# Optimization experiments

Hardware: AMD Instinct MI355X
Metric: run time of the kernel (lower is better)

## Reference

```python
import jax, jax.numpy as jnp
import numpy as np

N = 512
H = 128
L = 4
NUM_RBF = 50
CUTOFF = 5.0
NMOL = 16
OUT = 1


def setup_inputs() -> dict:
    key = jax.random.key(0)
    ks = jax.random.split(key, 12)
    s = lambda f: 1.0 / np.sqrt(f)
    atomic_numbers = jax.random.randint(ks[0], (N,), 0, 100)
    positions = jax.random.normal(ks[1], (N, 3), dtype=jnp.float32) * 2.0
    batch = jnp.sort(jax.random.randint(ks[2], (N,), 0, NMOL))
    return {
        'atomic_numbers': atomic_numbers,
        'positions': positions,
        'batch': batch,
        'embed': jax.random.normal(ks[3], (100, H), dtype=jnp.float32) * 0.1,
        'msg_w1': jax.random.normal(ks[4], (L, H + NUM_RBF + 3, H), dtype=jnp.float32) * s(H + NUM_RBF + 3),
        'msg_b1': jnp.zeros((L, H), jnp.float32),
        'msg_w2': jax.random.normal(ks[5], (L, H, H), dtype=jnp.float32) * s(H),
        'msg_b2': jnp.zeros((L, H), jnp.float32),
        'upd_w1': jax.random.normal(ks[6], (L, 2 * H, H), dtype=jnp.float32) * s(2 * H),
        'upd_b1': jnp.zeros((L, H), jnp.float32),
        'upd_w2': jax.random.normal(ks[7], (L, H, H), dtype=jnp.float32) * s(H),
        'upd_b2': jnp.zeros((L, H), jnp.float32),
        'out_w1': jax.random.normal(ks[8], (H, H // 2), dtype=jnp.float32) * s(H),
        'out_b1': jnp.zeros((H // 2,), jnp.float32),
        'out_w2': jax.random.normal(ks[9], (H // 2, OUT), dtype=jnp.float32) * s(H // 2),
        'out_b2': jnp.zeros((OUT,), jnp.float32),
    }


def _forward(atomic_numbers, positions, batch, embed, msg_w1, msg_b1, msg_w2,
             msg_b2, upd_w1, upd_b1, upd_w2, upd_b2, out_w1, out_b1, out_w2, out_b2):
    x = embed[jnp.clip(atomic_numbers, 0, 99)]                      # [N,H]
    # all-pairs geometry: row i = source, col j = target (matches repeat_interleave/repeat)
    diff = positions[:, None, :] - positions[None, :, :]            # [N,N,3]
    dist = jnp.linalg.norm(diff, axis=-1)                           # [N,N]
    not_self = jnp.arange(N)[:, None] != jnp.arange(N)[None, :]
    valid = (dist < CUTOFF) & not_self                              # [N,N] edge mask
    dirs = diff / jnp.maximum(dist, 1e-8)[..., None]                # [N,N,3]
    # gaussian RBF: centers linspace(0, cutoff, num_rbf), width = cutoff/num_rbf
    centers = jnp.linspace(0.0, CUTOFF, NUM_RBF)
    width = CUTOFF / NUM_RBF
    rbf = jnp.exp(-(dist[..., None] - centers) ** 2 / (2.0 * width ** 2))  # [N,N,50]

    for l in range(L):
        # Linear over concat([x_j, rbf, dirs]) split by input blocks (same math)
        Wx = msg_w1[l, :H]
        Wr = msg_w1[l, H:H + NUM_RBF]
        Wd = msg_w1[l, H + NUM_RBF:]
        pre = (x @ Wx)[:, None, :] \
            + jnp.einsum('ijr,rh->ijh', rbf, Wr) \
            + jnp.einsum('ijd,dh->ijh', dirs, Wd) + msg_b1[l]       # [N,N,H]
        m = jax.nn.silu(pre) @ msg_w2[l] + msg_b2[l]                # [N,N,H]
        m = jnp.where(valid[..., None], m, 0.0)
        aggr = m.sum(axis=0)                                        # scatter-add to target j
        upd_in = jnp.concatenate([x, aggr], axis=-1)                # [N,2H]
        x = x + jax.nn.silu(upd_in @ upd_w1[l] + upd_b1[l]) @ upd_w2[l] + upd_b2[l]

    # per-molecule mean pool
    sums = jax.ops.segment_sum(x, batch, num_segments=NMOL)         # [NMOL,H]
    counts = jax.ops.segment_sum(jnp.ones((N,), x.dtype), batch, num_segments=NMOL)
    pooled = sums / jnp.maximum(counts, 1.0)[:, None]
    return jax.nn.silu(pooled @ out_w1 + out_b1) @ out_w2 + out_b2  # [NMOL,OUT]


def reference(atomic_numbers, positions, batch, embed, msg_w1, msg_b1, msg_w2,
              msg_b2, upd_w1, upd_b1, upd_w2, upd_b2, out_w1, out_b1, out_w2, out_b2):
    return _forward(atomic_numbers, positions, batch, embed, msg_w1, msg_b1, msg_w2,
                    msg_b2, upd_w1, upd_b1, upd_w2, upd_b2, out_w1, out_b1, out_w2, out_b2)
```

## Files before the change

### kernel.cpp

```cpp
#include <hip/hip_runtime.h>
#include <math.h>

#define N 512
#define H 128
#define L 4
#define NUM_RBF 50
#define NMOL 16
#define SUPER 64
#define FSTRIDE 72

typedef __attribute__((ext_vector_type(8))) short short8;
typedef __attribute__((ext_vector_type(4))) float float4v;
typedef __attribute__((ext_vector_type(4))) int int4v;

__device__ __forceinline__ float silu_f(float v) {
    return v / (1.0f + __expf(-v));
}

__device__ __forceinline__ unsigned short f2bf(float f) {
    unsigned int u = __float_as_uint(f);
    unsigned int r = (u + 0x7FFFu + ((u >> 16) & 1u)) >> 16;
    return (unsigned short)r;
}

__global__ __launch_bounds__(512) void k_embed_lin(const int* __restrict__ an,
                                                   const float* __restrict__ embed,
                                                   const float* __restrict__ pos,
                                                   const float* __restrict__ wx,
                                                   const float* __restrict__ b1,
                                                   float* __restrict__ x,
                                                   float* __restrict__ a,
                                                   int* __restrict__ nbr,
                                                   int* __restrict__ ncnt) {
    int j = blockIdx.x;
    int tid = threadIdx.x;
    int lane = tid & 63;
    int wave = tid >> 6;
    int h = tid & 127;
    int grp = tid >> 7;

    __shared__ float xs[H];
    __shared__ int wsum8[8];
    __shared__ float part[4][H];

    float pjx = pos[j * 3 + 0], pjy = pos[j * 3 + 1], pjz = pos[j * 3 + 2];

    if (tid < H) {
        int z = an[j];
        z = min(max(z, 0), 99);
        float xv = embed[z * H + tid];
        xs[tid] = xv;
        x[j * H + tid] = xv;
    }

    {
        int i = tid;
        float dx = pos[i * 3 + 0] - pjx;
        float dy = pos[i * 3 + 1] - pjy;
        float dz = pos[i * 3 + 2] - pjz;
        float d2 = dx * dx + dy * dy + dz * dz;
        int valid = (d2 < 25.0f) && (i != j);
        unsigned long long m = __ballot(valid);
        int pre = __popcll(m & ((1ull << lane) - 1ull));
        if (lane == 0) wsum8[wave] = __popcll(m);
        __syncthreads();
        int wbase = 0, total = 0;
        for (int w = 0; w < 8; w++) {
            if (w < wave) wbase += wsum8[w];
            total += wsum8[w];
        }
        if (valid) nbr[j * 512 + wbase + pre] = i;
        int padded = (total + 63) & ~63;
        for (int s = total + tid; s < padded; s += 512) nbr[j * 512 + s] = j;
        if (tid == 0) ncnt[j] = total;
    }

    {
        float p0 = 0.f, p1 = 0.f, p2 = 0.f, p3 = 0.f;
        int k0 = grp * 32;
#pragma unroll 8
        for (int k = 0; k < 32; k += 4) {
            p0 += xs[k0 + k]     * wx[(k0 + k)     * H + h];
            p1 += xs[k0 + k + 1] * wx[(k0 + k + 1) * H + h];
            p2 += xs[k0 + k + 2] * wx[(k0 + k + 2) * H + h];
            p3 += xs[k0 + k + 3] * wx[(k0 + k + 3) * H + h];
        }
        part[grp][h] = (p0 + p1) + (p2 + p3);
    }
    __syncthreads();
    if (grp == 0)
        a[j * H + h] = part[0][h] + part[1][h] + part[2][h] + part[3][h] + b1[h];
}

__global__ __launch_bounds__(512) void k_layer(const float* __restrict__ a,
                                               const float* __restrict__ pos,
                                               const int* __restrict__ nbr,
                                               const int* __restrict__ ncnt,
                                               const float* __restrict__ wfeat,
                                               const float* __restrict__ w2,
                                               const float* __restrict__ b2,
                                               const float* __restrict__ u1,
                                               const float* __restrict__ ub1,
                                               const float* __restrict__ u2,
                                               const float* __restrict__ ub2,
                                               float* __restrict__ x,
                                               const float* __restrict__ wxn,
                                               const float* __restrict__ b1n,
                                               float* __restrict__ a_next) {
    int j = blockIdx.x;
    int tid = threadIdx.x;
    int g = tid >> 8;
    int t8 = tid & 255;
    int lane = tid & 63;
    int wv4 = (tid >> 6) & 3;
    int nn = lane & 15;
    int quad = lane >> 4;
    int hbase = wv4 * 32;

    __shared__ unsigned short F[2][2][SUPER * FSTRIDE];
    __shared__ int nidx[2][2][SUPER];
    __shared__ float sjp[2][H];
    __shared__ float sj[H], xj[H], ag[H], hid[H], xn[H];
    __shared__ float part[4][H];

    int cnt = ncnt[j];
    float pjx = pos[j * 3 + 0], pjy = pos[j * 3 + 1], pjz = pos[j * 3 + 2];

    if (tid < 2 * H) sjp[tid >> 7][tid & 127] = 0.0f;
    if (tid < H) xj[tid] = x[j * H + tid];

    short8 bfrag[2][2];
    for (int c = 0; c < 2; c++) {
        for (int t = 0; t < 2; t++) {
            short8 b;
            int h = hbase + 16 * t + nn;
#pragma unroll
            for (int jj = 0; jj < 8; jj++) {
                int k = c * 32 + quad * 8 + jj;
                float v = (k < NUM_RBF + 3) ? wfeat[k * H + h] : 0.0f;
                b[jj] = (short)f2bf(v);
            }
            bfrag[c][t] = b;
        }
    }

    const float DELTA = 5.0f / 49.0f;
    float pacc0 = 0.0f, pacc1 = 0.0f;

    int S = (cnt + 63) >> 6;
    int rounds = (S + 1) >> 1;

    int il = t8 >> 2;
    int kb = (t8 & 3) * 16;

    auto stage = [&](int s, int b) {
        int ni = nbr[j * 512 + s * 64 + il];
        if ((t8 & 3) == 0) nidx[g][b][il] = ni;
        float dx = pos[ni * 3 + 0] - pjx;
        float dy = pos[ni * 3 + 1] - pjy;
        float dz = pos[ni * 3 + 2] - pjz;
        float d = sqrtf(dx * dx + dy * dy + dz * dz);
        float rinv = 1.0f / fmaxf(d, 1e-8f);
        unsigned short vals[16];
#pragma unroll
        for (int qq = 0; qq < 16; qq++) {
            int k = kb + qq;
            float v;
            if (k < NUM_RBF) {
                float tt = d - (float)k * DELTA;
                v = __expf(-50.0f * tt * tt);
            } else if (k == NUM_RBF)     v = dx * rinv;
            else if (k == NUM_RBF + 1)   v = dy * rinv;
            else if (k == NUM_RBF + 2)   v = dz * rinv;
            else                         v = 0.0f;
            vals[qq] = f2bf(v);
        }
        unsigned int* dst = (unsigned int*)&F[g][b][il * FSTRIDE + kb];
#pragma unroll
        for (int qq = 0; qq < 8; qq++)
            dst[qq] = (unsigned int)vals[2 * qq] | ((unsigned int)vals[2 * qq + 1] << 16);
    };

    if (g < S) stage(g, 0);
    __syncthreads();

    for (int r = 0; r < rounds; r++) {
        int s = 2 * r + g;
        int sn = 2 * (r + 1) + g;
        if (sn < S) stage(sn, (r + 1) & 1);
        if (s < S) {
            int b = r & 1;
#pragma unroll
            for (int it = 0; it < SUPER / 16; it++) {
                int lbase = it * 16 + quad * 4;
                int4v ni4 = *(const int4v*)&nidx[g][b][lbase];
                float av0[4], av1[4];
#pragma unroll
                for (int rr = 0; rr < 4; rr++) {
                    av0[rr] = a[ni4[rr] * H + hbase + nn];
                    av1[rr] = a[ni4[rr] * H + hbase + 16 + nn];
                }
                short8 afrag0 = *(const short8*)&F[g][b][(it * 16 + nn) * FSTRIDE + 0 * 32 + quad * 8];
                short8 afrag1 = *(const short8*)&F[g][b][(it * 16 + nn) * FSTRIDE + 1 * 32 + quad * 8];
                float4v acc0 = {0.0f, 0.0f, 0.0f, 0.0f};
                float4v acc1 = {0.0f, 0.0f, 0.0f, 0.0f};
                acc0 = __builtin_amdgcn_mfma_f32_16x16x32_bf16(afrag0, bfrag[0][0], acc0, 0, 0, 0);
                acc0 = __builtin_amdgcn_mfma_f32_16x16x32_bf16(afrag1, bfrag[1][0], acc0, 0, 0, 0);
                acc1 = __builtin_amdgcn_mfma_f32_16x16x32_bf16(afrag0, bfrag[0][1], acc1, 0, 0, 0);
                acc1 = __builtin_amdgcn_mfma_f32_16x16x32_bf16(afrag1, bfrag[1][1], acc1, 0, 0, 0);
#pragma unroll
                for (int rr = 0; rr < 4; rr++) {
                    float vm = (s * 64 + lbase + rr < cnt) ? 1.0f : 0.0f;
                    pacc0 += vm * silu_f(acc0[rr] + av0[rr]);
                    pacc1 += vm * silu_f(acc1[rr] + av1[rr]);
                }
            }
        }
        __syncthreads();
    }

    pacc0 += __shfl_xor(pacc0, 16, 64);
    pacc0 += __shfl_xor(pacc0, 32, 64);
    pacc1 += __shfl_xor(pacc1, 16, 64);
    pacc1 += __shfl_xor(pacc1, 32, 64);
    if (lane < 16) {
        sjp[g][hbase + lane]      = pacc0;
        sjp[g][hbase + 16 + lane] = pacc1;
    }
    __syncthreads();
    if (tid < H) sj[tid] = sjp[0][tid] + sjp[1][tid];
    __syncthreads();

    int h = tid & 127;
    int grp = tid >> 7;

    {
        float p0 = 0.f, p1 = 0.f, p2 = 0.f, p3 = 0.f;
        int k0 = grp * 32;
#pragma unroll 8
        for (int k = 0; k < 32; k += 4) {
            p0 += sj[k0 + k]     * w2[(k0 + k)     * H + h];
            p1 += sj[k0 + k + 1] * w2[(k0 + k + 1) * H + h];
            p2 += sj[k0 + k + 2] * w2[(k0 + k + 2) * H + h];
            p3 += sj[k0 + k + 3] * w2[(k0 + k + 3) * H + h];
        }
        part[grp][h] = (p0 + p1) + (p2 + p3);
    }
    __syncthreads();
    if (grp == 0) ag[h] = part[0][h] + part[1][h] + part[2][h] + part[3][h] + (float)cnt * b2[h];
    __syncthreads();

    {
        const float* src = (grp < 2) ? xj : ag;
        int sbase = (grp & 1) * 64;
        int k0 = grp * 64;
        float p0 = 0.f, p1 = 0.f, p2 = 0.f, p3 = 0.f;
#pragma unroll 8
        for (int k = 0; k < 64; k += 4) {
            p0 += src[sbase + k]     * u1[(k0 + k)     * H + h];
            p1 += src[sbase + k + 1] * u1[(k0 + k + 1) * H + h];
            p2 += src[sbase + k + 2] * u1[(k0 + k + 2) * H + h];
            p3 += src[sbase + k + 3] * u1[(k0 + k + 3) * H + h];
        }
        part[grp][h] = (p0 + p1) + (p2 + p3);
    }
    __syncthreads();
    if (grp == 0) hid[h] = silu_f(part[0][h] + part[1][h] + part[2][h] + part[3][h] + ub1[h]);
    __syncthreads();

    {
        float p0 = 0.f, p1 = 0.f, p2 = 0.f, p3 = 0.f;
        int k0 = grp * 32;
#pragma unroll 8
        for (int k = 0; k < 32; k += 4) {
            p0 += hid[k0 + k]     * u2[(k0 + k)     * H + h];
            p1 += hid[k0 + k + 1] * u2[(k0 + k + 1) * H + h];
            p2 += hid[k0 + k + 2] * u2[(k0 + k + 2) * H + h];
            p3 += hid[k0 + k + 3] * u2[(k0 + k + 3) * H + h];
        }
        part[grp][h] = (p0 + p1) + (p2 + p3);
    }
    __syncthreads();
    if (grp == 0) {
        float xv = xj[h] + part[0][h] + part[1][h] + part[2][h] + part[3][h] + ub2[h];
        x[j * H + h] = xv;
        xn[h] = xv;
    }

    if (a_next != nullptr) {
        __syncthreads();
        float p0 = 0.f, p1 = 0.f, p2 = 0.f, p3 = 0.f;
        int k0 = grp * 32;
#pragma unroll 8
        for (int k = 0; k < 32; k += 4) {
            p0 += xn[k0 + k]     * wxn[(k0 + k)     * H + h];
            p1 += xn[k0 + k + 1] * wxn[(k0 + k + 1) * H + h];
            p2 += xn[k0 + k + 2] * wxn[(k0 + k + 2) * H + h];
            p3 += xn[k0 + k + 3] * wxn[(k0 + k + 3) * H + h];
        }
        part[grp][h] = (p0 + p1) + (p2 + p3);
        __syncthreads();
        if (grp == 0)
            a_next[j * H + h] = part[0][h] + part[1][h] + part[2][h] + part[3][h] + b1n[h];
    }
}

__global__ __launch_bounds__(H) void k_pool(const float* __restrict__ x,
                                            const int* __restrict__ batch,
                                            const float* __restrict__ ow1,
                                            const float* __restrict__ ob1,
                                            const float* __restrict__ ow2,
                                            const float* __restrict__ ob2,
                                            float* __restrict__ out) {
    int m = blockIdx.x;
    int h = threadIdx.x;
    __shared__ int lo_s, hi_s;
    __shared__ float pooled[H];
    __shared__ float hid[H / 2];

    if (h == 0) {
        int a = 0, b = N;
        while (a < b) { int mid = (a + b) >> 1; if (batch[mid] < m) a = mid + 1; else b = mid; }
        lo_s = a;
        b = N;
        while (a < b) { int mid = (a + b) >> 1; if (batch[mid] < m + 1) a = mid + 1; else b = mid; }
        hi_s = a;
    }
    __syncthreads();

    int lo = lo_s, hi = hi_s;
    float s = 0.0f;
    for (int i = lo; i < hi; i++) s += x[i * H + h];
    pooled[h] = s / (float)max(hi - lo, 1);
    __syncthreads();

    if (h < H / 2) {
        float p0 = 0.f, p1 = 0.f;
        for (int k = 0; k < H; k += 2) {
            p0 += pooled[k]     * ow1[(k)     * (H / 2) + h];
            p1 += pooled[k + 1] * ow1[(k + 1) * (H / 2) + h];
        }
        hid[h] = silu_f(p0 + p1 + ob1[h]);
    }
    __syncthreads();

    if (h == 0) {
        float o = ob2[0];
        for (int k = 0; k < H / 2; k++) o += hid[k] * ow2[k];
        out[m] = o;
    }
}

extern "C" void kernel_launch(void* const* d_in, const int* in_sizes, int n_in,
                              void* d_out, int out_size, void* d_ws, size_t ws_size,
                              hipStream_t stream) {
    const int*   an      = (const int*)d_in[0];
    const float* pos     = (const float*)d_in[1];
    const int*   batch   = (const int*)d_in[2];
    const float* embed   = (const float*)d_in[3];
    const float* msg_w1  = (const float*)d_in[4];
    const float* msg_b1  = (const float*)d_in[5];
    const float* msg_w2  = (const float*)d_in[6];
    const float* msg_b2  = (const float*)d_in[7];
    const float* upd_w1  = (const float*)d_in[8];
    const float* upd_b1  = (const float*)d_in[9];
    const float* upd_w2  = (const float*)d_in[10];
    const float* upd_b2  = (const float*)d_in[11];
    const float* out_w1  = (const float*)d_in[12];
    const float* out_b1  = (const float*)d_in[13];
    const float* out_w2  = (const float*)d_in[14];
    const float* out_b2  = (const float*)d_in[15];
    float* out = (float*)d_out;

    float* x    = (float*)d_ws;
    float* a0   = x + N * H;
    float* a1   = a0 + N * H;
    int*   nbr  = (int*)(a1 + N * H);
    int*   ncnt = nbr + N * 512;

    const int W1ROWS = H + NUM_RBF + 3;

    k_embed_lin<<<N, 512, 0, stream>>>(an, embed, pos, msg_w1, msg_b1, x, a0, nbr, ncnt);
    for (int l = 0; l < L; l++) {
        float* a_cur  = (l & 1) ? a1 : a0;
        float* a_next = (l + 1 < L) ? ((l & 1) ? a0 : a1) : nullptr;
        const float* wxn = (l + 1 < L) ? (msg_w1 + (l + 1) * W1ROWS * H) : nullptr;
        const float* b1n = (l + 1 < L) ? (msg_b1 + (l + 1) * H) : nullptr;
        k_layer<<<N, 512, 0, stream>>>(a_cur, pos, nbr, ncnt,
                                       msg_w1 + l * W1ROWS * H + H * H,
                                       msg_w2 + l * H * H, msg_b2 + l * H,
                                       upd_w1 + l * 2 * H * H, upd_b1 + l * H,
                                       upd_w2 + l * H * H, upd_b2 + l * H,
                                       x, wxn, b1n, a_next);
    }
    k_pool<<<NMOL, H, 0, stream>>>(x, batch, out_w1, out_b1, out_w2, out_b2, out);
}
```

Baseline: 222.0 us.

## Precompute bf16 edge features once and stream tiles via global_load_lds

The RBF and direction features for each edge were recomputed in every layer kernel. They are now computed once in the embedding kernel and stored as swizzled bf16 tiles in the workspace, and each layer copies them into LDS asynchronously with global_load_lds. The neighbour index list is also loaded once per block, and the pool kernel splits its atom summation over four thread groups. This trades repeated exp work for extra global memory traffic of roughly 4 MB of tiles read per layer, and relies on the workspace being large enough.

```diff
diff --git a/kernel.cpp b/kernel.cpp
--- a/kernel.cpp
+++ b/kernel.cpp
@@ -7,7 +7,7 @@
 #define NUM_RBF 50
 #define NMOL 16
 #define SUPER 64
-#define FSTRIDE 72
+#define MAXS 8
 
 typedef __attribute__((ext_vector_type(8))) short short8;
 typedef __attribute__((ext_vector_type(4))) float float4v;
@@ -21,6 +21,12 @@
     unsigned int u = __float_as_uint(f);
     unsigned int r = (u + 0x7FFFu + ((u >> 16) & 1u)) >> 16;
     return (unsigned short)r;
+}
+
+__device__ __forceinline__ void gld_lds16(const void* g, void* l) {
+    __builtin_amdgcn_global_load_lds(
+        (const __attribute__((address_space(1))) unsigned int*)g,
+        (__attribute__((address_space(3))) unsigned int*)l, 16, 0, 0);
 }
 
 __global__ __launch_bounds__(512) void k_embed_lin(const int* __restrict__ an,
@@ -31,7 +37,8 @@
                                                    float* __restrict__ x,
                                                    float* __restrict__ a,
                                                    int* __restrict__ nbr,
-                                                   int* __restrict__ ncnt) {
+                                                   int* __restrict__ ncnt,
+                                                   unsigned short* __restrict__ Fg) {
     int j = blockIdx.x;
     int tid = threadIdx.x;
     int lane = tid & 63;
@@ -53,6 +60,7 @@
         x[j * H + tid] = xv;
     }
 
+    int padded;
     {
         int i = tid;
         float dx = pos[i * 3 + 0] - pjx;
@@ -70,7 +78,7 @@
             total += wsum8[w];
         }
         if (valid) nbr[j * 512 + wbase + pre] = i;
-        int padded = (total + 63) & ~63;
+        padded = (total + 63) & ~63;
         for (int s = total + tid; s < padded; s += 512) nbr[j * 512 + s] = j;
         if (tid == 0) ncnt[j] = total;
     }
@@ -90,12 +98,52 @@
     __syncthreads();
     if (grp == 0)
         a[j * H + h] = part[0][h] + part[1][h] + part[2][h] + part[3][h] + b1[h];
+
+    const float DELTA = 5.0f / 49.0f;
+    int kb = (tid & 3) * 16;
+#pragma unroll
+    for (int pass = 0; pass < 4; pass++) {
+        int slot = pass * 128 + (tid >> 2);
+        if (slot < padded) {
+            int ni = nbr[j * 512 + slot];
+            float dx = pos[ni * 3 + 0] - pjx;
+            float dy = pos[ni * 3 + 1] - pjy;
+            float dz = pos[ni * 3 + 2] - pjz;
+            float d = sqrtf(dx * dx + dy * dy + dz * dz);
+            float rinv = 1.0f / fmaxf(d, 1e-8f);
+            unsigned short vals[16];
+#pragma unroll
+            for (int qq = 0; qq < 16; qq++) {
+                int k = kb + qq;
+                float v;
+                if (k < NUM_RBF) {
+                    float tt = d - (float)k * DELTA;
+                    v = __expf(-50.0f * tt * tt);
+                } else if (k == NUM_RBF)     v = dx * rinv;
+                else if (k == NUM_RBF + 1)   v = dy * rinv;
+                else if (k == NUM_RBF + 2)   v = dz * rinv;
+                else                         v = 0.0f;
+                vals[qq] = f2bf(v);
+            }
+            int row = slot & 63;
+            unsigned short* tile = Fg + (((size_t)(j * MAXS + (slot >> 6))) << 12);
+            int c0 = kb >> 3;
+            int4v p0, p1;
+#pragma unroll
+            for (int q = 0; q < 4; q++) {
+                p0[q] = (int)((unsigned)vals[2 * q]     | ((unsigned)vals[2 * q + 1] << 16));
+                p1[q] = (int)((unsigned)vals[8 + 2 * q] | ((unsigned)vals[9 + 2 * q] << 16));
+            }
+            *(int4v*)(tile + row * 64 + (((c0    ) ^ (row & 7)) << 3)) = p0;
+            *(int4v*)(tile + row * 64 + (((c0 + 1) ^ (row & 7)) << 3)) = p1;
+        }
+    }
 }
 
 __global__ __launch_bounds__(512) void k_layer(const float* __restrict__ a,
-                                               const float* __restrict__ pos,
                                                const int* __restrict__ nbr,
                                                const int* __restrict__ ncnt,
+                                               const unsigned short* __restrict__ Fg,
                                                const float* __restrict__ wfeat,
                                                const float* __restrict__ w2,
                                                const float* __restrict__ b2,
@@ -110,24 +158,23 @@
     int j = blockIdx.x;
     int tid = threadIdx.x;
     int g = tid >> 8;
-    int t8 = tid & 255;
     int lane = tid & 63;
     int wv4 = (tid >> 6) & 3;
     int nn = lane & 15;
     int quad = lane >> 4;
     int hbase = wv4 * 32;
 
-    __shared__ unsigned short F[2][2][SUPER * FSTRIDE];
-    __shared__ int nidx[2][2][SUPER];
+    __shared__ __align__(16) unsigned short F[2][2][SUPER * 64];
+    __shared__ __align__(16) int nidx_all[512];
     __shared__ float sjp[2][H];
     __shared__ float sj[H], xj[H], ag[H], hid[H], xn[H];
     __shared__ float part[4][H];
 
     int cnt = ncnt[j];
-    float pjx = pos[j * 3 + 0], pjy = pos[j * 3 + 1], pjz = pos[j * 3 + 2];
 
     if (tid < 2 * H) sjp[tid >> 7][tid & 127] = 0.0f;
     if (tid < H) xj[tid] = x[j * H + tid];
+    nidx_all[tid] = nbr[j * 512 + tid];
 
     short8 bfrag[2][2];
     for (int c = 0; c < 2; c++) {
@@ -144,64 +191,44 @@
         }
     }
 
-    const float DELTA = 5.0f / 49.0f;
-    float pacc0 = 0.0f, pacc1 = 0.0f;
-
     int S = (cnt + 63) >> 6;
     int rounds = (S + 1) >> 1;
 
-    int il = t8 >> 2;
-    int kb = (t8 & 3) * 16;
-
-    auto stage = [&](int s, int b) {
-        int ni = nbr[j * 512 + s * 64 + il];
-        if ((t8 & 3) == 0) nidx[g][b][il] = ni;
-        float dx = pos[ni * 3 + 0] - pjx;
-        float dy = pos[ni * 3 + 1] - pjy;
-        float dz = pos[ni * 3 + 2] - pjz;
-        float d = sqrtf(dx * dx + dy * dy + dz * dz);
-        float rinv = 1.0f / fmaxf(d, 1e-8f);
-        unsigned short vals[16];
-#pragma unroll
-        for (int qq = 0; qq < 16; qq++) {
-            int k = kb + qq;
-            float v;
-            if (k < NUM_RBF) {
-                float tt = d - (float)k * DELTA;
-                v = __expf(-50.0f * tt * tt);
-            } else if (k == NUM_RBF)     v = dx * rinv;
-            else if (k == NUM_RBF + 1)   v = dy * rinv;
-            else if (k == NUM_RBF + 2)   v = dz * rinv;
-            else                         v = 0.0f;
-            vals[qq] = f2bf(v);
-        }
-        unsigned int* dst = (unsigned int*)&F[g][b][il * FSTRIDE + kb];
-#pragma unroll
-        for (int qq = 0; qq < 8; qq++)
-            dst[qq] = (unsigned int)vals[2 * qq] | ((unsigned int)vals[2 * qq + 1] << 16);
+    auto stage_tile = [&](int s, int b) {
+        const char* src = (const char*)(Fg + (((size_t)(j * MAXS + s)) << 12));
+        char* dst = (char*)&F[g][b][0];
+#pragma unroll
+        for (int q = 0; q < 2; q++) {
+            int off = (wv4 + 4 * q) << 10;
+            gld_lds16(src + off + lane * 16, dst + off);
+        }
     };
 
-    if (g < S) stage(g, 0);
-    __syncthreads();
+    if (g < S) stage_tile(g, 0);
+    __syncthreads();
+
+    float pacc0 = 0.0f, pacc1 = 0.0f;
 
     for (int r = 0; r < rounds; r++) {
         int s = 2 * r + g;
         int sn = 2 * (r + 1) + g;
-        if (sn < S) stage(sn, (r + 1) & 1);
+        if (sn < S) stage_tile(sn, (r + 1) & 1);
         if (s < S) {
-            int b = r & 1;
+            int cur = r & 1;
 #pragma unroll
             for (int it = 0; it < SUPER / 16; it++) {
                 int lbase = it * 16 + quad * 4;
-                int4v ni4 = *(const int4v*)&nidx[g][b][lbase];
+                int4v ni4 = *(const int4v*)&nidx_all[s * 64 + lbase];
                 float av0[4], av1[4];
 #pragma unroll
                 for (int rr = 0; rr < 4; rr++) {
                     av0[rr] = a[ni4[rr] * H + hbase + nn];
                     av1[rr] = a[ni4[rr] * H + hbase + 16 + nn];
                 }
-                short8 afrag0 = *(const short8*)&F[g][b][(it * 16 + nn) * FSTRIDE + 0 * 32 + quad * 8];
-                short8 afrag1 = *(const short8*)&F[g][b][(it * 16 + nn) * FSTRIDE + 1 * 32 + quad * 8];
+                int row = it * 16 + nn;
+                const char* fb = (const char*)&F[g][cur][0] + row * 128;
+                short8 afrag0 = *(const short8*)(fb + ((quad       ^ (row & 7)) << 4));
+                short8 afrag1 = *(const short8*)(fb + (((quad + 4) ^ (row & 7)) << 4));
                 float4v acc0 = {0.0f, 0.0f, 0.0f, 0.0f};
                 float4v acc1 = {0.0f, 0.0f, 0.0f, 0.0f};
                 acc0 = __builtin_amdgcn_mfma_f32_16x16x32_bf16(afrag0, bfrag[0][0], acc0, 0, 0, 0);
@@ -305,20 +332,23 @@
     }
 }
 
-__global__ __launch_bounds__(H) void k_pool(const float* __restrict__ x,
-                                            const int* __restrict__ batch,
-                                            const float* __restrict__ ow1,
-                                            const float* __restrict__ ob1,
-                                            const float* __restrict__ ow2,
-                                            const float* __restrict__ ob2,
-                                            float* __restrict__ out) {
+__global__ __launch_bounds__(512) void k_pool(const float* __restrict__ x,
+                                              const int* __restrict__ batch,
+                                              const float* __restrict__ ow1,
+                                              const float* __restrict__ ob1,
+                                              const float* __restrict__ ow2,
+                                              const float* __restrict__ ob2,
+                                              float* __restrict__ out) {
     int m = blockIdx.x;
-    int h = threadIdx.x;
+    int tid = threadIdx.x;
+    int h = tid & 127;
+    int q = tid >> 7;
     __shared__ int lo_s, hi_s;
+    __shared__ float psum[4][H];
     __shared__ float pooled[H];
     __shared__ float hid[H / 2];
 
-    if (h == 0) {
+    if (tid == 0) {
         int a = 0, b = N;
         while (a < b) { int mid = (a + b) >> 1; if (batch[mid] < m) a = mid + 1; else b = mid; }
         lo_s = a;
@@ -330,11 +360,13 @@
 
     int lo = lo_s, hi = hi_s;
     float s = 0.0f;
-    for (int i = lo; i < hi; i++) s += x[i * H + h];
-    pooled[h] = s / (float)max(hi - lo, 1);
-    __syncthreads();
-
-    if (h < H / 2) {
+    for (int i = lo + q; i < hi; i += 4) s += x[i * H + h];
+    psum[q][h] = s;
+    __syncthreads();
+    if (q == 0) pooled[h] = (psum[0][h] + psum[1][h] + psum[2][h] + psum[3][h]) / (float)max(hi - lo, 1);
+    __syncthreads();
+
+    if (tid < H / 2) {
         float p0 = 0.f, p1 = 0.f;
         for (int k = 0; k < H; k += 2) {
             p0 += pooled[k]     * ow1[(k)     * (H / 2) + h];
@@ -344,7 +376,7 @@
     }
     __syncthreads();
 
-    if (h == 0) {
+    if (tid == 0) {
         float o = ob2[0];
         for (int k = 0; k < H / 2; k++) o += hid[k] * ow2[k];
         out[m] = o;
@@ -377,21 +409,22 @@
     float* a1   = a0 + N * H;
     int*   nbr  = (int*)(a1 + N * H);
     int*   ncnt = nbr + N * 512;
+    unsigned short* Fg = (unsigned short*)(ncnt + N);
 
     const int W1ROWS = H + NUM_RBF + 3;
 
-    k_embed_lin<<<N, 512, 0, stream>>>(an, embed, pos, msg_w1, msg_b1, x, a0, nbr, ncnt);
+    k_embed_lin<<<N, 512, 0, stream>>>(an, embed, pos, msg_w1, msg_b1, x, a0, nbr, ncnt, Fg);
     for (int l = 0; l < L; l++) {
         float* a_cur  = (l & 1) ? a1 : a0;
         float* a_next = (l + 1 < L) ? ((l & 1) ? a0 : a1) : nullptr;
         const float* wxn = (l + 1 < L) ? (msg_w1 + (l + 1) * W1ROWS * H) : nullptr;
         const float* b1n = (l + 1 < L) ? (msg_b1 + (l + 1) * H) : nullptr;
-        k_layer<<<N, 512, 0, stream>>>(a_cur, pos, nbr, ncnt,
+        k_layer<<<N, 512, 0, stream>>>(a_cur, nbr, ncnt, Fg,
                                        msg_w1 + l * W1ROWS * H + H * H,
                                        msg_w2 + l * H * H, msg_b2 + l * H,
                                        upd_w1 + l * 2 * H * H, upd_b1 + l * H,
                                        upd_w2 + l * H * H, upd_b2 + l * H,
                                        x, wxn, b1n, a_next);
     }
-    k_pool<<<NMOL, H, 0, stream>>>(x, batch, out_w1, out_b1, out_w2, out_b2, out);
-}
+    k_pool<<<NMOL, 512, 0, stream>>>(x, batch, out_w1, out_b1, out_w2, out_b2, out);
+}
```

Result: faster. 215.8 us (-2.8%).
